# Kernel tuning notes

Measured on AMD Instinct MI355X. Metric: run time of the kernel, lower is better.

## Reference

```python
import jax, jax.numpy as jnp
import numpy as np

B, N, D, L, H, DH, M, FF = 4, 2048, 512, 6, 8, 64, 266, 2048
EPS_LN = 1e-5
KERNEL_EPS = 1e-4


def fixed_pos_emb(n, dim):
    # performer_pytorch FixedPositionalEmbedding: cat(sin, cos) over half-dims
    inv_freq = 1.0 / (10000.0 ** (jnp.arange(0, dim, 2, dtype=jnp.float32) / dim))
    t = jnp.arange(n, dtype=jnp.float32)
    s = jnp.einsum('i,j->ij', t, inv_freq)  # [n, dim//2]
    return jnp.concatenate([jnp.sin(s), jnp.cos(s)], axis=-1)  # [n, dim]


def layer_norm(x, g, b):
    mu = x.mean(-1, keepdims=True)
    var = ((x - mu) ** 2).mean(-1, keepdims=True)
    return (x - mu) * jax.lax.rsqrt(var + EPS_LN) * g + b


def rotate_every_two(t):
    t1 = t[..., ::2]
    t2 = t[..., 1::2]
    return jnp.stack([-t2, t1], axis=-1).reshape(t.shape)


def apply_rotary(q, k, sinu):
    # sinu: [n, DH] = cat(sin_half, cos_half); repeat each value twice (interleaved)
    half = sinu.shape[-1] // 2
    sin = jnp.repeat(sinu[:, :half], 2, axis=-1)  # [n, DH]
    cos = jnp.repeat(sinu[:, half:], 2, axis=-1)
    q = q * cos + rotate_every_two(q) * sin
    k = k * cos + rotate_every_two(k) * sin
    return q, k


def softmax_kernel(data, proj, is_query):
    # data: [B,H,N,DH], proj: [M,DH]
    d = data.shape[-1]
    data_normalizer = d ** -0.25
    ratio = proj.shape[0] ** -0.5
    data_dash = jnp.einsum('bhnd,md->bhnm', data * data_normalizer, proj)
    diag = (data ** 2).sum(-1) * 0.5 * (data_normalizer ** 2)  # [B,H,N]
    if is_query:
        m = jnp.max(data_dash, axis=-1, keepdims=True)
    else:
        m = jnp.max(data_dash)
    return ratio * (jnp.exp(data_dash - diag[..., None] - m) + KERNEL_EPS)


def linear_attention(qf, kf, v):
    # qf/kf: [B,H,N,M], v: [B,H,N,DH]  (non-causal FAVOR+)
    k_sum = kf.sum(axis=-2)  # [B,H,M]
    d_inv = 1.0 / jnp.einsum('bhnm,bhm->bhn', qf, k_sum)
    context = jnp.einsum('bhnm,bhne->bhme', kf, v)  # [B,H,M,DH]
    return jnp.einsum('bhme,bhnm,bhn->bhne', context, qf, d_inv)


def setup_inputs() -> dict:
    key = jax.random.key(0)
    ks = jax.random.split(key, 8)
    std = 0.02
    inp = {
        'x': jax.random.normal(ks[0], (B, N, D), jnp.float32),
        'Wq': jax.random.normal(ks[1], (L, D, H * DH), jnp.float32) * std,
        'Wk': jax.random.normal(ks[2], (L, D, H * DH), jnp.float32) * std,
        'Wv': jax.random.normal(ks[3], (L, D, H * DH), jnp.float32) * std,
        'Wo': jax.random.normal(ks[4], (L, H * DH, D), jnp.float32) * std,
        'proj': jax.random.normal(ks[5], (L, M, DH), jnp.float32),
        'ln1_g': jnp.ones((L, D), jnp.float32),
        'ln1_b': jnp.zeros((L, D), jnp.float32),
        'W1': jax.random.normal(ks[6], (L, D, FF), jnp.float32) * std,
        'b1': jnp.zeros((L, FF), jnp.float32),
        'W2': jax.random.normal(ks[7], (L, FF, D), jnp.float32) * std,
        'b2': jnp.zeros((L, D), jnp.float32),
        'ln2_g': jnp.ones((L, D), jnp.float32),
        'ln2_b': jnp.zeros((L, D), jnp.float32),
        'lnf_g': jnp.ones((D,), jnp.float32),
        'lnf_b': jnp.zeros((D,), jnp.float32),
    }
    return inp


def reference(x, Wq, Wk, Wv, Wo, proj, ln1_g, ln1_b, W1, b1, W2, b2, ln2_g, ln2_b, lnf_g, lnf_b):
    n = x.shape[1]
    x = x + fixed_pos_emb(n, D)[None]          # additive sinusoidal emb
    sinu = fixed_pos_emb(n, DH)                 # per-head rotary table [n, DH]
    for i in range(L):
        # --- PreLayerNorm FAVOR+ self-attention ---
        h = layer_norm(x, ln1_g[i], ln1_b[i])
        q = jnp.einsum('bnd,de->bne', h, Wq[i]).reshape(B, n, H, DH).transpose(0, 2, 1, 3)
        k = jnp.einsum('bnd,de->bne', h, Wk[i]).reshape(B, n, H, DH).transpose(0, 2, 1, 3)
        v = jnp.einsum('bnd,de->bne', h, Wv[i]).reshape(B, n, H, DH).transpose(0, 2, 1, 3)
        q, k = apply_rotary(q, k, sinu)
        qf = softmax_kernel(q, proj[i], True)
        kf = softmax_kernel(k, proj[i], False)
        o = linear_attention(qf, kf, v)         # [B,H,n,DH]
        o = o.transpose(0, 2, 1, 3).reshape(B, n, H * DH)
        x = x + jnp.einsum('bne,ed->bnd', o, Wo[i])
        # --- PreLayerNorm FFN (GELU) ---
        h = layer_norm(x, ln2_g[i], ln2_b[i])
        h = jax.nn.gelu(jnp.einsum('bnd,df->bnf', h, W1[i]) + b1[i], approximate=False)
        x = x + jnp.einsum('bnf,fd->bnd', h, W2[i]) + b2[i]
    return layer_norm(x, lnf_g, lnf_b)
```

## Files before the change

kernel.cpp:

```cpp
#include <hip/hip_runtime.h>
#include <hip/hip_bf16.h>
#include <cstdint>

typedef float v4f __attribute__((ext_vector_type(4)));
typedef short v8s __attribute__((ext_vector_type(8)));
typedef unsigned short u16;

#define N_SEQ 2048
#define D_MODEL 512
#define N_LAYER 6
#define N_HEAD 8
#define D_HEAD 64
#define M_FEAT 266
#define M_PAD 288
#define M_ALLOC 384
#define FF_DIM 2048
#define BATCH 4
#define ROWS 8192
#define BHN 65536

__device__ __forceinline__ float b2f(u16 u) {
  return __uint_as_float(((uint32_t)u) << 16);
}
__device__ __forceinline__ u16 f2b(float f) {
  union { __hip_bfloat16 h; u16 u; } c;
  c.h = __float2bfloat16(f);
  return c.u;
}
__device__ __forceinline__ float wave_sum(float v) {
#pragma unroll
  for (int o = 1; o < 64; o <<= 1) v += __shfl_xor(v, o);
  return v;
}
__device__ __forceinline__ float wave_max(float v) {
#pragma unroll
  for (int o = 1; o < 64; o <<= 1) v = fmaxf(v, __shfl_xor(v, o));
  return v;
}

__device__ __forceinline__ float gelu_f(float x) {
  float ax = fabsf(x) * 0.70710678118f;
  float tt = __builtin_amdgcn_rcpf(fmaf(0.3275911f, ax, 1.0f));
  float poly = tt * fmaf(tt, fmaf(tt, fmaf(tt, fmaf(tt, 1.061405429f, -1.453152027f),
                                           1.421413741f), -0.284496736f), 0.254829592f);
  float er = 1.0f - poly * __expf(-ax * ax);
  er = copysignf(er, x);
  return 0.5f * x * (1.0f + er);
}

__device__ __forceinline__ void mfma_bf16(v4f& d, v8s a, v8s b) {
  asm volatile("v_mfma_f32_16x16x32_bf16 %0, %1, %2, %0" : "+v"(d) : "v"(a), "v"(b));
}

__device__ __forceinline__ void async16(const u16* g, u16* l) {
  __builtin_amdgcn_global_load_lds(
      (const __attribute__((address_space(1))) uint32_t*)g,
      (__attribute__((address_space(3))) uint32_t*)l, 16, 0, 0);
}

template <int EPI, int KSPLIT>
__global__ void __launch_bounds__(512, 4)
gemm3s(const u16* __restrict__ A, const u16* __restrict__ B,
       void* __restrict__ Cv, const float* __restrict__ bias,
       int K, int ldc)
{
  extern __shared__ u16 lds[];
  const int t = threadIdx.x;
  const int lane = t & 63;
  const int w = t >> 6;
  const int wm = w >> 2;
  const int wn = w & 3;
  const int tiM = blockIdx.x << 7, tiN = blockIdx.y << 8;
  const int ks = (KSPLIT > 1) ? blockIdx.z : 0;
  const int kchunk = K / KSPLIT;
  const int NT = kchunk >> 5;

  const int rr = lane & 15;
  const int kq = (lane >> 4) << 3;
  const int sw = ((rr >> 1) & 3) << 3;
  const int cr = kq ^ sw;

  const int srow = t >> 2;
  const int scol = (((t & 3) ^ ((srow >> 1) & 3)) << 3);
  const u16* Abase = A + (long long)(tiM + srow) * K + scol + (long long)ks * kchunk;
  const u16* Bbase = B + (long long)(tiN + srow) * K + scol + (long long)ks * kchunk;
  const long long r128 = 128LL * K;

  v4f acc[4][4] = {};

  auto stage3 = [&](int s, int kt) {
    const long long k0 = (long long)kt * 32;
    u16* d = &lds[s * 12288 + t * 8];
    async16(Abase + k0, d);
    async16(Bbase + k0, d + 4096);
    async16(Bbase + k0 + r128, d + 8192);
  };

  stage3(0, 0);
  stage3(1, 1);
  asm volatile("s_waitcnt vmcnt(3)" ::: "memory");
  __builtin_amdgcn_s_barrier();

  for (int kt = 0; kt < NT; ++kt) {
    const int s = kt % 3;
    const int sp = (kt + 2) % 3;
    const bool st = (kt + 2 < NT);
    const int ab = s * 12288;
    const int bb = ab + 4096;
    v8s af[4], bf[4];
#pragma unroll
    for (int i = 0; i < 4; i++) {
      af[i] = *(const v8s*)&lds[ab + (wm * 64 + i * 16 + rr) * 32 + cr];
      bf[i] = *(const v8s*)&lds[bb + (wn * 64 + i * 16 + rr) * 32 + cr];
    }
    if (st) stage3(sp, kt + 2);
    __builtin_amdgcn_s_setprio(1);
#pragma unroll
    for (int m = 0; m < 4; m++)
#pragma unroll
      for (int n = 0; n < 4; n++) mfma_bf16(acc[m][n], af[m], bf[n]);
    __builtin_amdgcn_s_setprio(0);
    if (st) asm volatile("s_waitcnt vmcnt(3)" ::: "memory");
    else    asm volatile("s_waitcnt vmcnt(0)" ::: "memory");
    __builtin_amdgcn_s_barrier();
  }

  __builtin_amdgcn_sched_barrier(0);
  asm volatile("s_nop 7\ns_nop 7\ns_nop 7");
  __builtin_amdgcn_sched_barrier(0);

  const int r4 = (lane >> 4) << 2;
  const int cc = lane & 15;
#pragma unroll
  for (int mf = 0; mf < 4; mf++)
#pragma unroll
    for (int nf = 0; nf < 4; nf++)
#pragma unroll
      for (int i = 0; i < 4; i++) {
        int row = tiM + wm * 64 + mf * 16 + r4 + i;
        int col = tiN + wn * 64 + nf * 16 + cc;
        float v = acc[mf][nf][i];
        if (EPI == 0) {
          ((u16*)Cv)[(long long)row * ldc + col] = f2b(v);
        } else if (EPI == 3) {
          ((u16*)Cv)[(long long)row * ldc + col] = f2b(gelu_f(v + bias[col]));
        } else {
          ((float*)Cv)[((long long)ks * ROWS + row) * ldc + col] = v;
        }
      }
}

__global__ void ff2red(const float* __restrict__ part, const float* __restrict__ bias,
                       float* __restrict__ x)
{
  long long i = ((long long)blockIdx.x * 256 + threadIdx.x) * 8;
  int col = (int)(i & 511);
  v4f s0 = {}, s1 = {};
#pragma unroll
  for (int ks = 0; ks < 4; ks++) {
    const float* p = part + (long long)ks * (ROWS * 512LL) + i;
    s0 += *(const v4f*)p;
    s1 += *(const v4f*)(p + 4);
  }
  v4f b0 = *(const v4f*)(bias + col);
  v4f b1 = *(const v4f*)(bias + col + 4);
  v4f x0 = *(const v4f*)(x + i), x1 = *(const v4f*)(x + i + 4);
  x0 += s0 + b0;
  x1 += s1 + b1;
  *(v4f*)(x + i) = x0;
  *(v4f*)(x + i + 4) = x1;
}

template <int EPI, int BN, int KSPLIT>
__global__ void __launch_bounds__(256, 4)
gemm2(const u16* __restrict__ A, const u16* __restrict__ B,
      void* __restrict__ Cv, const float* __restrict__ bias,
      int K, int ldc, long long sA, long long sB, long long sC,
      float scale, int Ncap, int Mcap, unsigned int* __restrict__ gmax)
{
  __shared__ u16 As[2][128 * 32];
  __shared__ u16 Bs[2][BN * 32];
  __shared__ float smax[4];
  const int zz = blockIdx.z;
  const int z = (KSPLIT > 1) ? zz / KSPLIT : zz;
  const int ks = (KSPLIT > 1) ? zz % KSPLIT : 0;
  const int kchunk = K / KSPLIT;
  const u16* Ag = A + (long long)z * sA + ks * kchunk;
  const u16* Bg = B + (long long)z * sB + ks * kchunk;
  const int t = threadIdx.x;
  const int lane = t & 63;
  const int w = t >> 6;
  constexpr int NF = BN / 32;
  const int wm = (w >> 1) << 6;
  const int wn = (w & 1) * (BN / 2);
  const int tiM = blockIdx.x << 7, tiN = blockIdx.y * BN;

  const int srow = t >> 2;
  const int scol = (t & 3) << 3;
  const u16* Ap = Ag + (long long)(tiM + srow) * K + scol;
  const u16* Bp = Bg + (long long)(tiN + srow) * K + scol;
  const long long rstride = 64LL * K;

  const int rr = lane & 15;
  const int kc = (lane >> 4) << 3;

  v4f acc[4][NF] = {};

  const int nk = kchunk >> 5;
  auto stage = [&](int buf, int k0) {
    async16(Ap + k0, &As[buf][t * 8]);
    async16(Ap + k0 + rstride, &As[buf][t * 8 + 2048]);
    async16(Bp + k0, &Bs[buf][t * 8]);
    if (BN == 128) async16(Bp + k0 + rstride, &Bs[buf][t * 8 + 2048]);
  };

  stage(0, 0);
  __syncthreads();
  int cur = 0;
  for (int kt = 0; kt < nk; ++kt) {
    if (kt + 1 < nk) stage(cur ^ 1, (kt + 1) << 5);
    v8s af[4], bf[NF];
#pragma unroll
    for (int i = 0; i < 4; i++) af[i] = *(const v8s*)&As[cur][(wm + rr + i * 16) * 32 + kc];
#pragma unroll
    for (int i = 0; i < NF; i++) bf[i] = *(const v8s*)&Bs[cur][(wn + rr + i * 16) * 32 + kc];
#pragma unroll
    for (int fm = 0; fm < 4; fm++)
#pragma unroll
      for (int fn = 0; fn < NF; fn++)
        mfma_bf16(acc[fm][fn], af[fm], bf[fn]);
    __syncthreads();
    cur ^= 1;
  }

  __builtin_amdgcn_sched_barrier(0);
  asm volatile("s_nop 7\ns_nop 7\ns_nop 7");
  __builtin_amdgcn_sched_barrier(0);

  const int r4 = (lane >> 4) << 2;
  const int cc = lane & 15;
  float lmax = -3e38f;
#pragma unroll
  for (int fm = 0; fm < 4; fm++)
#pragma unroll
    for (int fn = 0; fn < NF; fn++)
#pragma unroll
      for (int i = 0; i < 4; i++) {
        int row = tiM + wm + fm * 16 + r4 + i;
        int col = tiN + wn + fn * 16 + cc;
        float v = acc[fm][fn][i];
        if (EPI == 5) {
          if (row < Mcap && col < Ncap)
            ((float*)Cv)[((long long)zz * M_ALLOC + row) * 64 + col] = v;
        } else if (EPI == 6) {
          float sv = v * scale;
          if (col < Ncap) ((float*)Cv)[(long long)row * ldc + col] = sv;
          if (col < M_FEAT) lmax = fmaxf(lmax, sv);
        }
      }

  if (EPI == 6) {
    lmax = wave_max(lmax);
    if (lane == 0) smax[w] = lmax;
    __syncthreads();
    if (t == 0) {
      float m = fmaxf(fmaxf(smax[0], smax[1]), fmaxf(smax[2], smax[3]));
      unsigned int u = __float_as_uint(m);
      unsigned int key = (u & 0x80000000u) ? ~u : (u | 0x80000000u);
      atomicMax(gmax, key);
    }
  }
}

template <int EPI>
__global__ void __launch_bounds__(256, 6)
gemm_small(const u16* __restrict__ A, const u16* __restrict__ B,
           void* __restrict__ Cv, const float* __restrict__ bias,
           int K, int ldc, long long sA, long long sB)
{
  __shared__ u16 As[2][64 * 32];
  __shared__ u16 Bs[2][64 * 32];
  const int z = blockIdx.z;
  const u16* Ag = A + (long long)z * sA;
  const u16* Bg = B + (long long)z * sB;
  const int t = threadIdx.x;
  const int lane = t & 63;
  const int w = t >> 6;
  const int wm = (w >> 1) << 5;
  const int wn = (w & 1) << 5;
  const int tiM = blockIdx.x << 6, tiN = blockIdx.y << 6;

  const int srow = t >> 2;
  const int scol = (t & 3) << 3;
  const u16* Ap = Ag + (long long)(tiM + srow) * K + scol;
  const u16* Bp = Bg + (long long)(tiN + srow) * K + scol;

  const int rr = lane & 15;
  const int kc = (lane >> 4) << 3;

  v4f acc[2][2] = {};

  const int nk = K >> 5;
  auto stage = [&](int buf, int k0) {
    async16(Ap + k0, &As[buf][t * 8]);
    async16(Bp + k0, &Bs[buf][t * 8]);
  };

  stage(0, 0);
  __syncthreads();
  int cur = 0;
  for (int kt = 0; kt < nk; ++kt) {
    if (kt + 1 < nk) stage(cur ^ 1, (kt + 1) << 5);
    v8s af[2], bf[2];
#pragma unroll
    for (int i = 0; i < 2; i++) af[i] = *(const v8s*)&As[cur][(wm + rr + i * 16) * 32 + kc];
#pragma unroll
    for (int i = 0; i < 2; i++) bf[i] = *(const v8s*)&Bs[cur][(wn + rr + i * 16) * 32 + kc];
#pragma unroll
    for (int fm = 0; fm < 2; fm++)
#pragma unroll
      for (int fn = 0; fn < 2; fn++)
        mfma_bf16(acc[fm][fn], af[fm], bf[fn]);
    __syncthreads();
    cur ^= 1;
  }

  __builtin_amdgcn_sched_barrier(0);
  asm volatile("s_nop 7\ns_nop 7\ns_nop 7");
  __builtin_amdgcn_sched_barrier(0);

  const int r4 = (lane >> 4) << 2;
  const int cc = lane & 15;
#pragma unroll
  for (int fm = 0; fm < 2; fm++)
#pragma unroll
    for (int fn = 0; fn < 2; fn++)
#pragma unroll
      for (int i = 0; i < 4; i++) {
        int row = tiM + wm + fm * 16 + r4 + i;
        int col = tiN + wn + fn * 16 + cc;
        float v = acc[fm][fn][i];
        if (EPI == 0) {
          ((u16*)Cv)[(long long)row * ldc + col] = f2b(v);
        } else if (EPI == 2) {
          long long idx = (long long)row * ldc + col;
          float bb = bias ? bias[col] : 0.0f;
          ((float*)Cv)[idx] += v + bb;
        } else if (EPI == 3) {
          ((u16*)Cv)[(long long)row * ldc + col] = f2b(gelu_f(v + bias[col]));
        } else {
          int b_ = z >> 3, h_ = z & 7;
          ((u16*)Cv)[(long long)(b_ * N_SEQ + row) * 512 + h_ * 64 + col] = f2b(v);
        }
      }
}

__global__ void __launch_bounds__(384, 3)
ddq_qf(const u16* __restrict__ qr, const u16* __restrict__ proj,
       const float* __restrict__ diag, const float* __restrict__ ksum,
       u16* __restrict__ qf)
{
  __shared__ u16 As[2][64 * 32];
  __shared__ u16 Bs[2][288 * 32];
  __shared__ float redw[6][64];
  __shared__ float rowv[64];
  __shared__ float sdg[64];
  const int bh = blockIdx.z;
  const int tiM = blockIdx.x << 6;
  const int t = threadIdx.x;
  const int lane = t & 63;
  const int w = t >> 6;
  const u16* Ag = qr + (long long)bh * (N_SEQ * 64);
  const int srow = t >> 2, scol = (t & 3) << 3;
  const u16* Ap = Ag + (long long)(tiM + srow) * 64 + scol;
  const int rr = lane & 15, kc = (lane >> 4) << 3;
  const int wn = w * 48;

  if (t < 64) sdg[t] = diag[(long long)bh * N_SEQ + tiM + t];

  v4f acc[4][3] = {};
  auto stage = [&](int buf, int k0) {
    if (t < 256) async16(Ap + k0, &As[buf][t * 8]);
#pragma unroll
    for (int j = 0; j < 3; j++) {
      int idx = j * 384 + t;
      async16(proj + (long long)(idx >> 2) * 64 + ((idx & 3) << 3) + k0,
              &Bs[buf][j * 3072 + t * 8]);
    }
  };

  stage(0, 0);
  __syncthreads();
  for (int kt = 0; kt < 2; ++kt) {
    if (kt == 0) stage(1, 32);
    v8s af[4], bf[3];
#pragma unroll
    for (int i = 0; i < 4; i++) af[i] = *(const v8s*)&As[kt][(rr + i * 16) * 32 + kc];
#pragma unroll
    for (int i = 0; i < 3; i++) bf[i] = *(const v8s*)&Bs[kt][(wn + i * 16 + rr) * 32 + kc];
#pragma unroll
    for (int fm = 0; fm < 4; fm++)
#pragma unroll
      for (int fn = 0; fn < 3; fn++)
        mfma_bf16(acc[fm][fn], af[fm], bf[fn]);
    __syncthreads();
  }

  __builtin_amdgcn_sched_barrier(0);
  asm volatile("s_nop 7\ns_nop 7\ns_nop 7");
  __builtin_amdgcn_sched_barrier(0);

  const int r4 = (lane >> 4) << 2;
  const int cc = lane & 15;
  const float sc = 0.35355339f;

#pragma unroll
  for (int fm = 0; fm < 4; fm++)
#pragma unroll
    for (int i = 0; i < 4; i++) {
      float m = -3e38f;
#pragma unroll
      for (int fn = 0; fn < 3; fn++) {
        int col = wn + fn * 16 + cc;
        float v = acc[fm][fn][i] * sc;
        if (col < M_FEAT) m = fmaxf(m, v);
      }
#pragma unroll
      for (int o = 1; o < 16; o <<= 1) m = fmaxf(m, __shfl_xor(m, o));
      if (cc == 0) redw[w][fm * 16 + r4 + i] = m;
    }
  __syncthreads();
  if (t < 64) {
    float g = redw[0][t];
#pragma unroll
    for (int ww = 1; ww < 6; ww++) g = fmaxf(g, redw[ww][t]);
    rowv[t] = g;
  }
  __syncthreads();

  float ksv[3];
#pragma unroll
  for (int fn = 0; fn < 3; fn++) ksv[fn] = ksum[bh * M_PAD + wn + fn * 16 + cc];

#pragma unroll
  for (int fm = 0; fm < 4; fm++)
#pragma unroll
    for (int i = 0; i < 4; i++) {
      int row = fm * 16 + r4 + i;
      float gm = rowv[row];
      float dg = sdg[row];
      float s = 0.0f;
#pragma unroll
      for (int fn = 0; fn < 3; fn++) {
        float e = 0.06131389f * (expf(acc[fm][fn][i] * sc - dg - gm) + 1e-4f);
        acc[fm][fn][i] = e;
        s += e * ksv[fn];
      }
#pragma unroll
      for (int o = 1; o < 16; o <<= 1) s += __shfl_xor(s, o);
      if (cc == 0) redw[w][row] = s;
    }
  __syncthreads();
  if (t < 64) {
    float s = redw[0][t];
#pragma unroll
    for (int ww = 1; ww < 6; ww++) s += redw[ww][t];
    rowv[t] = 1.0f / s;
  }
  __syncthreads();

#pragma unroll
  for (int fm = 0; fm < 4; fm++)
#pragma unroll
    for (int i = 0; i < 4; i++) {
      int row = fm * 16 + r4 + i;
      float dinv = rowv[row];
#pragma unroll
      for (int fn = 0; fn < 3; fn++) {
        int col = wn + fn * 16 + cc;
        qf[((long long)bh * N_SEQ + tiM + row) * M_PAD + col] =
            f2b(acc[fm][fn][i] * dinv);
      }
    }
}

template <bool F32OUT>
__global__ void ln_kernel(const float* __restrict__ x, const float* __restrict__ g,
                          const float* __restrict__ b, void* __restrict__ out)
{
  const int row = blockIdx.x * 4 + (threadIdx.x >> 6);
  const int lane = threadIdx.x & 63;
  const float* xr = x + (long long)row * D_MODEL + lane * 8;
  v4f v0 = *(const v4f*)xr;
  v4f v1 = *(const v4f*)(xr + 4);
  float s = v0[0] + v0[1] + v0[2] + v0[3] + v1[0] + v1[1] + v1[2] + v1[3];
  float sq = v0[0]*v0[0] + v0[1]*v0[1] + v0[2]*v0[2] + v0[3]*v0[3]
           + v1[0]*v1[0] + v1[1]*v1[1] + v1[2]*v1[2] + v1[3]*v1[3];
  s = wave_sum(s);
  sq = wave_sum(sq);
  float mu = s * (1.0f / D_MODEL);
  float var = sq * (1.0f / D_MODEL) - mu * mu;
  float rstd = rsqrtf(var + 1e-5f);
  v4f g0 = *(const v4f*)(g + lane * 8), g1 = *(const v4f*)(g + lane * 8 + 4);
  v4f bb0 = *(const v4f*)(b + lane * 8), bb1 = *(const v4f*)(b + lane * 8 + 4);
  float y[8];
#pragma unroll
  for (int j = 0; j < 4; j++) y[j] = (v0[j] - mu) * rstd * g0[j] + bb0[j];
#pragma unroll
  for (int j = 0; j < 4; j++) y[4 + j] = (v1[j] - mu) * rstd * g1[j] + bb1[j];
  if (F32OUT) {
    float* op = (float*)out + (long long)row * D_MODEL + lane * 8;
    v4f o0 = {y[0], y[1], y[2], y[3]}, o1 = {y[4], y[5], y[6], y[7]};
    *(v4f*)op = o0;
    *(v4f*)(op + 4) = o1;
  } else {
    u16* op = (u16*)out + (long long)row * D_MODEL + lane * 8;
    alignas(16) u16 tmp[8];
#pragma unroll
    for (int j = 0; j < 8; j++) tmp[j] = f2b(y[j]);
    *(v8s*)op = *(v8s*)tmp;
  }
}

__global__ void posadd(const float* __restrict__ xin, float* __restrict__ x)
{
  long long i = (long long)blockIdx.x * 256 + threadIdx.x;
  int d = (int)(i & 511);
  int n = (int)((i >> 9) & 2047);
  int j = d & 255;
  float sarg = (float)n * expf(-0.035977892f * (float)j);
  float pe = (d < 256) ? sinf(sarg) : cosf(sarg);
  x[i] = xin[i] + pe;
}

__global__ void rotab(float* __restrict__ ts, float* __restrict__ tc)
{
  int i = blockIdx.x * 64 + threadIdx.x;
  int n = i >> 5, j = i & 31;
  float sarg = (float)n * expf(-0.28782314f * (float)j);
  float s, c;
  sincosf(sarg, &s, &c);
  ts[i] = s;
  tc[i] = c;
}

__global__ void rotary_kernel(const u16* __restrict__ qkv,
                              const float* __restrict__ ts, const float* __restrict__ tc,
                              u16* __restrict__ qr, u16* __restrict__ kr,
                              float* __restrict__ dq, float* __restrict__ dk)
{
  int bid = blockIdx.x * 4 + (threadIdx.x >> 6);
  int n = bid & 2047;
  int h = (bid >> 11) & 7;
  int b = bid >> 14;
  int lane = threadIdx.x & 63;
  long long src = ((long long)(b * N_SEQ + n)) * 1536 + h * 64 + lane;
  float qv = b2f(qkv[src]);
  float kv = b2f(qkv[src + 512]);
  int j = lane >> 1;
  float sn = ts[n * 32 + j], cn = tc[n * 32 + j];
  float qp = __shfl_xor(qv, 1), kp = __shfl_xor(kv, 1);
  float qrv = (lane & 1) ? (qv * cn + qp * sn) : (qv * cn - qp * sn);
  float krv = (lane & 1) ? (kv * cn + kp * sn) : (kv * cn - kp * sn);
  u16 qb = f2b(qrv), kb = f2b(krv);
  long long dst = ((long long)bid) * 64 + lane;
  qr[dst] = qb;
  kr[dst] = kb;
  float q2 = b2f(qb); q2 *= q2;
  float k2 = b2f(kb); k2 *= k2;
  q2 = wave_sum(q2);
  k2 = wave_sum(k2);
  if (lane == 0) { dq[bid] = q2 * 0.0625f; dk[bid] = k2 * 0.0625f; }
}

__global__ void vtrans(const u16* __restrict__ qkv, u16* __restrict__ vT)
{
  int bid = blockIdx.x;
  int nt = bid & 31;
  int h = (bid >> 5) & 7;
  int b = bid >> 8;
  __shared__ u16 st[64][72];
  int t = threadIdx.x;
  int r = t >> 2, c = (t & 3) << 4;
  long long src = ((long long)(b * N_SEQ + nt * 64 + r)) * 1536 + 1024 + h * 64 + c;
  *(v8s*)&st[r][c] = *(const v8s*)(qkv + src);
  *(v8s*)&st[r][c + 8] = *(const v8s*)(qkv + src + 8);
  __syncthreads();
  alignas(16) u16 tmp[16];
#pragma unroll
  for (int jj = 0; jj < 16; jj++) tmp[jj] = st[c + jj][r];
  long long dst = ((long long)((b * 8 + h) * 64 + r)) * N_SEQ + nt * 64 + c;
  *(v8s*)(vT + dst) = *(v8s*)&tmp[0];
  *(v8s*)(vT + dst + 8) = *(v8s*)&tmp[8];
}

__global__ void wtrans(const float* __restrict__ src, u16* __restrict__ dst,
                       int Ks, int Ns, long long sSrc, long long sDst)
{
  int l = blockIdx.z;
  src += (long long)l * sSrc;
  dst += (long long)l * sDst;
  int n0 = blockIdx.x << 6, k0 = blockIdx.y << 6;
  __shared__ float st[64][68];
  int t = threadIdx.x;
  int r = t >> 2, c = (t & 3) << 4;
  const float* sp = src + (long long)(k0 + r) * Ns + n0 + c;
#pragma unroll
  for (int jj = 0; jj < 16; jj += 4) *(v4f*)&st[r][c + jj] = *(const v4f*)(sp + jj);
  __syncthreads();
  alignas(16) u16 tmp[16];
#pragma unroll
  for (int jj = 0; jj < 16; jj++) tmp[jj] = f2b(st[c + jj][r]);
  u16* dp = dst + (long long)(n0 + r) * Ks + k0 + c;
  *(v8s*)(dp) = *(v8s*)&tmp[0];
  *(v8s*)(dp + 8) = *(v8s*)&tmp[8];
}

__global__ void projconv(const float* __restrict__ proj, u16* __restrict__ out)
{
  int i = blockIdx.x * 256 + threadIdx.x;
  int dh = i & 63;
  int m = (i >> 6) % M_ALLOC;
  int l = i / (M_ALLOC * 64);
  float v = (m < M_FEAT) ? proj[((long long)l * M_FEAT + m) * 64 + dh] : 0.0f;
  out[i] = f2b(v);
}

__global__ void resetmax(unsigned int* p) { *p = 0u; }

__global__ void kfprep(const float* __restrict__ dd, const float* __restrict__ diag,
                       const unsigned int* __restrict__ kmax,
                       u16* __restrict__ kfT, float* __restrict__ part)
{
  int ntile = blockIdx.x;
  int m0 = blockIdx.y << 6;
  int bh = blockIdx.z;
  int n0 = ntile << 6;
  __shared__ float st[64][65];
  unsigned int kk = kmax[0];
  float km = (kk & 0x80000000u) ? __uint_as_float(kk ^ 0x80000000u)
                                : __uint_as_float(~kk);
  int t = threadIdx.x;
  int r = t >> 2, c = (t & 3) << 4;
  const float* dp = dd + ((long long)bh * N_SEQ + n0 + r) * M_PAD + m0 + c;
  float dg = diag[(long long)bh * N_SEQ + n0 + r];
  float vals[16];
  if (m0 + c + 16 <= M_PAD) {
#pragma unroll
    for (int j = 0; j < 16; j += 4) *(v4f*)&vals[j] = *(const v4f*)(dp + j);
  } else {
#pragma unroll
    for (int j = 0; j < 16; j++) vals[j] = (m0 + c + j < M_PAD) ? dp[j] : 0.0f;
  }
#pragma unroll
  for (int j = 0; j < 16; j++) {
    int m = m0 + c + j;
    float e = (m < M_FEAT) ? 0.06131389f * (expf(vals[j] - dg - km) + 1e-4f) : 0.0f;
    st[r][c + j] = e;
  }
  __syncthreads();
  int mr = t >> 2, nc = (t & 3) << 4;
  float s = 0.0f;
  alignas(16) u16 tmp[16];
#pragma unroll
  for (int j = 0; j < 16; j++) {
    float e = st[nc + j][mr];
    s += e;
    tmp[j] = f2b(e);
  }
  s += __shfl_xor(s, 1);
  s += __shfl_xor(s, 2);
  int m = m0 + mr;
  if (m < M_PAD) {
    u16* op = kfT + ((long long)bh * M_ALLOC + m) * N_SEQ + n0 + nc;
    *(v8s*)op = *(v8s*)&tmp[0];
    *(v8s*)(op + 8) = *(v8s*)&tmp[8];
    if ((t & 3) == 0)
      part[((long long)bh * M_PAD + m) * 32 + ntile] = s;
  }
}

__global__ void ksumred(const float* __restrict__ part, float* __restrict__ ksum)
{
  int i = blockIdx.x * 256 + threadIdx.x;
  if (i >= 32 * M_PAD) return;
  const float* p = part + (long long)i * 32;
  float s = 0.0f;
#pragma unroll
  for (int j = 0; j < 32; j += 4) {
    v4f v = *(const v4f*)(p + j);
    s += v[0] + v[1] + v[2] + v[3];
  }
  ksum[i] = s;
}

__global__ void ctxred(const float* __restrict__ part, u16* __restrict__ ctxT)
{
  int bh = blockIdx.y;
  int m0 = blockIdx.x << 6;
  __shared__ float st[64][65];
  int t = threadIdx.x;
  int r = t >> 2, c = (t & 3) << 4;
  int m = m0 + r;
  v4f s[4] = {};
  if (m < M_PAD) {
    for (int ks = 0; ks < 8; ks++) {
      const float* p = part + (((long long)bh * 8 + ks) * M_ALLOC + m) * 64 + c;
#pragma unroll
      for (int j = 0; j < 4; j++) s[j] += *(const v4f*)(p + j * 4);
    }
  }
#pragma unroll
  for (int j = 0; j < 4; j++)
#pragma unroll
    for (int e = 0; e < 4; e++) st[r][c + j * 4 + e] = s[j][e];
  __syncthreads();
  int e = t >> 2, mc = (t & 3) << 4;
  if (m0 + mc < M_PAD) {
    alignas(16) u16 tmp[16];
#pragma unroll
    for (int j = 0; j < 16; j++) tmp[j] = f2b(st[mc + j][e]);
    u16* op = ctxT + ((long long)bh * 64 + e) * M_PAD + m0 + mc;
    *(v8s*)op = *(v8s*)&tmp[0];
    *(v8s*)(op + 8) = *(v8s*)&tmp[8];
  }
}

extern "C" void kernel_launch(void* const* d_in, const int* in_sizes, int n_in,
                              void* d_out, int out_size, void* d_ws, size_t ws_size,
                              hipStream_t stream)
{
  const float* x_in = (const float*)d_in[0];
  const float* Wq  = (const float*)d_in[1];
  const float* Wk  = (const float*)d_in[2];
  const float* Wv  = (const float*)d_in[3];
  const float* Wo  = (const float*)d_in[4];
  const float* Pr  = (const float*)d_in[5];
  const float* ln1g = (const float*)d_in[6];
  const float* ln1b = (const float*)d_in[7];
  const float* W1  = (const float*)d_in[8];
  const float* b1  = (const float*)d_in[9];
  const float* W2  = (const float*)d_in[10];
  const float* b2  = (const float*)d_in[11];
  const float* ln2g = (const float*)d_in[12];
  const float* ln2b = (const float*)d_in[13];
  const float* lnfg = (const float*)d_in[14];
  const float* lnfb = (const float*)d_in[15];

  hipFuncSetAttribute(reinterpret_cast<const void*>(&gemm3s<0, 1>),
                      hipFuncAttributeMaxDynamicSharedMemorySize, 73728);
  hipFuncSetAttribute(reinterpret_cast<const void*>(&gemm3s<3, 1>),
                      hipFuncAttributeMaxDynamicSharedMemorySize, 73728);
  hipFuncSetAttribute(reinterpret_cast<const void*>(&gemm3s<5, 4>),
                      hipFuncAttributeMaxDynamicSharedMemorySize, 73728);

  char* ws = (char*)d_ws;
  size_t off = 0;
  auto alloc = [&](size_t bytes) -> void* {
    void* p = ws + off;
    off = (off + bytes + 255) & ~(size_t)255;
    return p;
  };

  float* x      = (float*)alloc((size_t)ROWS * D_MODEL * 4);
  float* tsin   = (float*)alloc((size_t)N_SEQ * 32 * 4);
  float* tcos   = (float*)alloc((size_t)N_SEQ * 32 * 4);
  u16*   wqkvT  = (u16*)alloc((size_t)N_LAYER * 1536 * 512 * 2);
  u16*   woT    = (u16*)alloc((size_t)N_LAYER * 512 * 512 * 2);
  u16*   w1T    = (u16*)alloc((size_t)N_LAYER * 2048 * 512 * 2);
  u16*   w2T    = (u16*)alloc((size_t)N_LAYER * 512 * 2048 * 2);
  u16*   projT  = (u16*)alloc((size_t)N_LAYER * M_ALLOC * 64 * 2);
  u16*   hbuf   = (u16*)alloc((size_t)ROWS * D_MODEL * 2);
  u16*   obuf   = (u16*)alloc((size_t)ROWS * D_MODEL * 2);
  float* big    = (float*)alloc((size_t)32 * N_SEQ * M_PAD * 4);
  u16*   qrbuf  = (u16*)alloc((size_t)BHN * 64 * 2);
  u16*   krbuf  = (u16*)alloc((size_t)BHN * 64 * 2);
  u16*   vTbuf  = (u16*)alloc((size_t)BHN * 64 * 2);
  float* diagq  = (float*)alloc((size_t)BHN * 4);
  float* diagk  = (float*)alloc((size_t)BHN * 4);
  unsigned int* kmaxu = (unsigned int*)alloc(256);
  u16*   kfT    = (u16*)alloc((size_t)32 * M_ALLOC * N_SEQ * 2);
  float* part   = (float*)alloc((size_t)32 * 8 * M_ALLOC * 64 * 4);
  float* kspart = (float*)alloc((size_t)32 * M_PAD * 32 * 4);
  u16*   ctxT   = (u16*)alloc((size_t)32 * 64 * M_PAD * 2);
  float* ksum   = (float*)alloc((size_t)32 * M_PAD * 4);
  (void)alloc(1 << 20);
  (void)ws_size; (void)in_sizes; (void)n_in; (void)out_size;
  float* ff2part = (float*)kfT;

  posadd<<<16384, 256, 0, stream>>>(x_in, x);
  rotab<<<1024, 64, 0, stream>>>(tsin, tcos);
  wtrans<<<dim3(8, 8, 6), 256, 0, stream>>>(Wq, wqkvT, 512, 512, 512LL * 512, 1536LL * 512);
  wtrans<<<dim3(8, 8, 6), 256, 0, stream>>>(Wk, wqkvT + 512LL * 512, 512, 512, 512LL * 512, 1536LL * 512);
  wtrans<<<dim3(8, 8, 6), 256, 0, stream>>>(Wv, wqkvT + 1024LL * 512, 512, 512, 512LL * 512, 1536LL * 512);
  wtrans<<<dim3(8, 8, 6), 256, 0, stream>>>(Wo, woT, 512, 512, 512LL * 512, 512LL * 512);
  wtrans<<<dim3(32, 8, 6), 256, 0, stream>>>(W1, w1T, 512, 2048, 512LL * 2048, 2048LL * 512);
  wtrans<<<dim3(8, 32, 6), 256, 0, stream>>>(W2, w2T, 2048, 512, 2048LL * 512, 512LL * 2048);
  projconv<<<(N_LAYER * M_ALLOC * 64) / 256, 256, 0, stream>>>(Pr, projT);

  for (int l = 0; l < N_LAYER; l++) {
    const u16* wq = wqkvT + (long long)l * 1536 * 512;
    const u16* wo = woT + (long long)l * 512 * 512;
    const u16* w1 = w1T + (long long)l * 2048 * 512;
    const u16* w2 = w2T + (long long)l * 512 * 2048;
    const u16* pj = projT + (long long)l * M_ALLOC * 64;

    resetmax<<<1, 1, 0, stream>>>(kmaxu);
    ln_kernel<false><<<ROWS / 4, 256, 0, stream>>>(x, ln1g + l * 512, ln1b + l * 512, hbuf);
    gemm3s<0, 1><<<dim3(64, 6), 512, 73728, stream>>>(hbuf, wq, big, nullptr, 512, 1536);
    rotary_kernel<<<BHN / 4, 256, 0, stream>>>((u16*)big, tsin, tcos, qrbuf, krbuf, diagq, diagk);
    vtrans<<<1024, 256, 0, stream>>>((u16*)big, vTbuf);
    gemm2<6, 128, 1><<<dim3(512, 3, 1), 256, 0, stream>>>(krbuf, pj, big, nullptr,
        64, M_PAD, 0, 0, 0, 0.35355339f, M_PAD, BHN, kmaxu);
    kfprep<<<dim3(32, 5, 32), 256, 0, stream>>>(big, diagk, kmaxu, kfT, kspart);
    ksumred<<<(32 * M_PAD + 255) / 256, 256, 0, stream>>>(kspart, ksum);
    gemm2<5, 64, 8><<<dim3(3, 1, 256), 256, 0, stream>>>(kfT, vTbuf, part, nullptr,
        2048, 64, (long long)M_ALLOC * N_SEQ, 64LL * N_SEQ, 0, 1.0f, 64, M_PAD, nullptr);
    ctxred<<<dim3(5, 32), 256, 0, stream>>>(part, ctxT);
    ddq_qf<<<dim3(32, 1, 32), 384, 0, stream>>>(qrbuf, pj, diagq, ksum, kfT);
    gemm_small<4><<<dim3(32, 1, 32), 256, 0, stream>>>(kfT, ctxT, obuf, nullptr,
        M_PAD, 0, (long long)N_SEQ * M_PAD, 64LL * M_PAD);
    gemm_small<2><<<dim3(128, 8, 1), 256, 0, stream>>>(obuf, wo, x, nullptr,
        512, 512, 0, 0);
    ln_kernel<false><<<ROWS / 4, 256, 0, stream>>>(x, ln2g + l * 512, ln2b + l * 512, hbuf);
    gemm3s<3, 1><<<dim3(64, 8), 512, 73728, stream>>>(hbuf, w1, big, b1 + (long long)l * 2048,
        512, 2048);
    gemm3s<5, 4><<<dim3(64, 2, 4), 512, 73728, stream>>>((u16*)big, w2, ff2part, nullptr,
        2048, 512);
    ff2red<<<2048, 256, 0, stream>>>(ff2part, b2 + (long long)l * 512, x);
  }

  ln_kernel<true><<<ROWS / 4, 256, 0, stream>>>(x, lnfg, lnfb, d_out);
}
```

Measured before the change: 1.549 ms.

## Recompute key projection in fused kf kernel instead of storing fp32 data_dash

```diff
diff --git a/kernel.cpp b/kernel.cpp
--- a/kernel.cpp
+++ b/kernel.cpp
@@ -252,14 +252,12 @@
         if (EPI == 5) {
           if (row < Mcap && col < Ncap)
             ((float*)Cv)[((long long)zz * M_ALLOC + row) * 64 + col] = v;
-        } else if (EPI == 6) {
-          float sv = v * scale;
-          if (col < Ncap) ((float*)Cv)[(long long)row * ldc + col] = sv;
-          if (col < M_FEAT) lmax = fmaxf(lmax, sv);
+        } else if (EPI == 7) {
+          if (col < M_FEAT) lmax = fmaxf(lmax, v * scale);
         }
       }
 
-  if (EPI == 6) {
+  if (EPI == 7) {
     lmax = wave_max(lmax);
     if (lane == 0) smax[w] = lmax;
     __syncthreads();
@@ -270,6 +268,100 @@
       atomicMax(gmax, key);
     }
   }
+}
+
+__global__ void __launch_bounds__(384, 3)
+kf_gemm(const u16* __restrict__ kr, const u16* __restrict__ proj,
+        const float* __restrict__ diagk, const unsigned int* __restrict__ kmax,
+        u16* __restrict__ kfT, float* __restrict__ part)
+{
+  __shared__ u16 As[2][288 * 32];
+  __shared__ u16 Bs[2][64 * 32];
+  __shared__ float sdg[64];
+  const int ntile = blockIdx.x;
+  const int bh = blockIdx.z;
+  const int n0 = ntile << 6;
+  const int t = threadIdx.x;
+  const int lane = t & 63;
+  const int w = t >> 6;
+  const u16* Bg = kr + (long long)bh * (N_SEQ * 64) + (long long)n0 * 64;
+  const int rr = lane & 15, kc = (lane >> 4) << 3;
+
+  if (t < 64) sdg[t] = diagk[(long long)bh * N_SEQ + n0 + t];
+  unsigned int kk = kmax[0];
+  const float km = (kk & 0x80000000u) ? __uint_as_float(kk ^ 0x80000000u)
+                                      : __uint_as_float(~kk);
+
+  v4f acc[3][4] = {};
+  auto stage = [&](int buf, int k0) {
+#pragma unroll
+    for (int j = 0; j < 3; j++) {
+      int idx = j * 384 + t;
+      async16(proj + (long long)(idx >> 2) * 64 + ((idx & 3) << 3) + k0,
+              &As[buf][j * 3072 + t * 8]);
+    }
+    if (t < 256) async16(Bg + (long long)(t >> 2) * 64 + ((t & 3) << 3) + k0,
+                         &Bs[buf][t * 8]);
+  };
+
+  stage(0, 0);
+  __syncthreads();
+  for (int kt = 0; kt < 2; ++kt) {
+    if (kt == 0) stage(1, 32);
+    v8s af[3], bf[4];
+#pragma unroll
+    for (int i = 0; i < 3; i++) af[i] = *(const v8s*)&As[kt][(w * 48 + i * 16 + rr) * 32 + kc];
+#pragma unroll
+    for (int i = 0; i < 4; i++) bf[i] = *(const v8s*)&Bs[kt][(i * 16 + rr) * 32 + kc];
+#pragma unroll
+    for (int fm = 0; fm < 3; fm++)
+#pragma unroll
+      for (int fn = 0; fn < 4; fn++)
+        mfma_bf16(acc[fm][fn], af[fm], bf[fn]);
+    __syncthreads();
+  }
+
+  __builtin_amdgcn_sched_barrier(0);
+  asm volatile("s_nop 7\ns_nop 7\ns_nop 7");
+  __builtin_amdgcn_sched_barrier(0);
+
+  const int r4 = (lane >> 4) << 2;
+  const int cc = lane & 15;
+  const float sc = 0.35355339f;
+
+#pragma unroll
+  for (int fm = 0; fm < 3; fm++)
+#pragma unroll
+    for (int i = 0; i < 4; i++) {
+      int m = w * 48 + fm * 16 + r4 + i;
+      float s = 0.0f;
+#pragma unroll
+      for (int fn = 0; fn < 4; fn++) {
+        float dd = acc[fm][fn][i] * sc;
+        float kf = (m < M_FEAT)
+            ? 0.06131389f * (__expf(dd - sdg[fn * 16 + cc] - km) + 1e-4f) : 0.0f;
+        acc[fm][fn][i] = kf;
+        s += kf;
+        kfT[((long long)bh * M_ALLOC + m) * N_SEQ + n0 + fn * 16 + cc] = f2b(kf);
+      }
+#pragma unroll
+      for (int o = 1; o < 16; o <<= 1) s += __shfl_xor(s, o);
+      if (cc == 0) part[((long long)bh * M_PAD + m) * 32 + ntile] = s;
+    }
+}
+
+__global__ void ksumred(const float* __restrict__ part, float* __restrict__ ksum)
+{
+  int i = blockIdx.x * 256 + threadIdx.x;
+  if (i >= 32 * M_PAD) return;
+  const float* p = part + (long long)i * 32;
+  float s = 0.0f;
+#pragma unroll
+  for (int j = 0; j < 32; j += 4) {
+    v4f v = *(const v4f*)(p + j);
+    s += v[0] + v[1] + v[2] + v[3];
+  }
+  ksum[i] = s;
 }
 
 template <int EPI>
@@ -340,14 +432,10 @@
         int row = tiM + wm + fm * 16 + r4 + i;
         int col = tiN + wn + fn * 16 + cc;
         float v = acc[fm][fn][i];
-        if (EPI == 0) {
-          ((u16*)Cv)[(long long)row * ldc + col] = f2b(v);
-        } else if (EPI == 2) {
+        if (EPI == 2) {
           long long idx = (long long)row * ldc + col;
           float bb = bias ? bias[col] : 0.0f;
           ((float*)Cv)[idx] += v + bb;
-        } else if (EPI == 3) {
-          ((u16*)Cv)[(long long)row * ldc + col] = f2b(gelu_f(v + bias[col]));
         } else {
           int b_ = z >> 3, h_ = z & 7;
           ((u16*)Cv)[(long long)(b_ * N_SEQ + row) * 512 + h_ * 64 + col] = f2b(v);
@@ -452,7 +540,7 @@
       float s = 0.0f;
 #pragma unroll
       for (int fn = 0; fn < 3; fn++) {
-        float e = 0.06131389f * (expf(acc[fm][fn][i] * sc - dg - gm) + 1e-4f);
+        float e = 0.06131389f * (__expf(acc[fm][fn][i] * sc - dg - gm) + 1e-4f);
         acc[fm][fn][i] = e;
         s += e * ksv[fn];
       }
@@ -627,72 +715,6 @@
 }
 
 __global__ void resetmax(unsigned int* p) { *p = 0u; }
-
-__global__ void kfprep(const float* __restrict__ dd, const float* __restrict__ diag,
-                       const unsigned int* __restrict__ kmax,
-                       u16* __restrict__ kfT, float* __restrict__ part)
-{
-  int ntile = blockIdx.x;
-  int m0 = blockIdx.y << 6;
-  int bh = blockIdx.z;
-  int n0 = ntile << 6;
-  __shared__ float st[64][65];
-  unsigned int kk = kmax[0];
-  float km = (kk & 0x80000000u) ? __uint_as_float(kk ^ 0x80000000u)
-                                : __uint_as_float(~kk);
-  int t = threadIdx.x;
-  int r = t >> 2, c = (t & 3) << 4;
-  const float* dp = dd + ((long long)bh * N_SEQ + n0 + r) * M_PAD + m0 + c;
-  float dg = diag[(long long)bh * N_SEQ + n0 + r];
-  float vals[16];
-  if (m0 + c + 16 <= M_PAD) {
-#pragma unroll
-    for (int j = 0; j < 16; j += 4) *(v4f*)&vals[j] = *(const v4f*)(dp + j);
-  } else {
-#pragma unroll
-    for (int j = 0; j < 16; j++) vals[j] = (m0 + c + j < M_PAD) ? dp[j] : 0.0f;
-  }
-#pragma unroll
-  for (int j = 0; j < 16; j++) {
-    int m = m0 + c + j;
-    float e = (m < M_FEAT) ? 0.06131389f * (expf(vals[j] - dg - km) + 1e-4f) : 0.0f;
-    st[r][c + j] = e;
-  }
-  __syncthreads();
-  int mr = t >> 2, nc = (t & 3) << 4;
-  float s = 0.0f;
-  alignas(16) u16 tmp[16];
-#pragma unroll
-  for (int j = 0; j < 16; j++) {
-    float e = st[nc + j][mr];
-    s += e;
-    tmp[j] = f2b(e);
-  }
-  s += __shfl_xor(s, 1);
-  s += __shfl_xor(s, 2);
-  int m = m0 + mr;
-  if (m < M_PAD) {
-    u16* op = kfT + ((long long)bh * M_ALLOC + m) * N_SEQ + n0 + nc;
-    *(v8s*)op = *(v8s*)&tmp[0];
-    *(v8s*)(op + 8) = *(v8s*)&tmp[8];
-    if ((t & 3) == 0)
-      part[((long long)bh * M_PAD + m) * 32 + ntile] = s;
-  }
-}
-
-__global__ void ksumred(const float* __restrict__ part, float* __restrict__ ksum)
-{
-  int i = blockIdx.x * 256 + threadIdx.x;
-  if (i >= 32 * M_PAD) return;
-  const float* p = part + (long long)i * 32;
-  float s = 0.0f;
-#pragma unroll
-  for (int j = 0; j < 32; j += 4) {
-    v4f v = *(const v4f*)(p + j);
-    s += v[0] + v[1] + v[2] + v[3];
-  }
-  ksum[i] = s;
-}
 
 __global__ void ctxred(const float* __restrict__ part, u16* __restrict__ ctxT)
 {
@@ -810,9 +832,9 @@
     gemm3s<0, 1><<<dim3(64, 6), 512, 73728, stream>>>(hbuf, wq, big, nullptr, 512, 1536);
     rotary_kernel<<<BHN / 4, 256, 0, stream>>>((u16*)big, tsin, tcos, qrbuf, krbuf, diagq, diagk);
     vtrans<<<1024, 256, 0, stream>>>((u16*)big, vTbuf);
-    gemm2<6, 128, 1><<<dim3(512, 3, 1), 256, 0, stream>>>(krbuf, pj, big, nullptr,
+    gemm2<7, 128, 1><<<dim3(512, 3, 1), 256, 0, stream>>>(krbuf, pj, nullptr, nullptr,
         64, M_PAD, 0, 0, 0, 0.35355339f, M_PAD, BHN, kmaxu);
-    kfprep<<<dim3(32, 5, 32), 256, 0, stream>>>(big, diagk, kmaxu, kfT, kspart);
+    kf_gemm<<<dim3(32, 1, 32), 384, 0, stream>>>(krbuf, pj, diagk, kmaxu, kfT, kspart);
     ksumred<<<(32 * M_PAD + 255) / 256, 256, 0, stream>>>(kspart, ksum);
     gemm2<5, 64, 8><<<dim3(3, 1, 256), 256, 0, stream>>>(kfT, vTbuf, part, nullptr,
         2048, 64, (long long)M_ALLOC * N_SEQ, 64LL * N_SEQ, 0, 1.0f, 64, M_PAD, nullptr);
```

New measurement: 1.474 ms. 4.8% less time.
